# Optimization experiments

Hardware: AMD Instinct MI355X
Metric: run time of the kernel (lower is better)

The kernel has to match this reference:

```python
import jax, jax.numpy as jnp
import numpy as np

NEG_SLOPE_ATT = 0.2   # DenseGATConv default negative_slope
NEG_SLOPE_OUT = 0.01  # F.leaky_relu default


def dense_gat_layer(x, adj, w, att_src, att_dst, bias, heads, concat):
    # x: [B, N, F_in], adj: [B, N, N] (0/1 float), w: [F_in, H*C]
    B, N, _ = x.shape
    h = (x @ w).reshape(B, N, heads, -1)                 # [B, N, H, C]
    a_src = jnp.einsum('bnhc,hc->bnh', h, att_src)       # [B, N, H]
    a_dst = jnp.einsum('bnhc,hc->bnh', h, att_dst)       # [B, N, H]
    # alpha[b,i,j,h] = a_src[b,j,h] + a_dst[b,i,h]
    alpha = a_src[:, None, :, :] + a_dst[:, :, None, :]  # [B, N, N, H]
    alpha = jax.nn.leaky_relu(alpha, NEG_SLOPE_ATT)
    alpha = jnp.where(adj[..., None] == 0, -jnp.inf, alpha)
    alpha = jax.nn.softmax(alpha, axis=2)                # over neighbors j
    out = jnp.einsum('bijh,bjhc->bihc', alpha, h)        # [B, N, H, C]
    if concat:
        out = out.reshape(B, N, -1)                      # [B, N, H*C]
    else:
        out = out.mean(axis=2)                           # [B, N, C]
    return out + bias


def setup_inputs() -> dict:
    key = jax.random.key(0)
    ks = jax.random.split(key, 9)
    B, N, F_IN, HID, H1, OUT = 1, 4096, 256, 64, 8, 128
    x = jax.random.normal(ks[0], (B, N, F_IN), dtype=jnp.float32)
    u = jax.random.uniform(ks[1], (B, N, N), dtype=jnp.float32)
    adj = (u < 0.05).astype(jnp.float32)
    eye = jnp.eye(N, dtype=jnp.float32)[None]
    adj = jnp.maximum(adj, eye)  # ensure self-loop so softmax rows are valid
    s1 = 1.0 / np.sqrt(F_IN)
    s2 = 1.0 / np.sqrt(HID * H1)
    return {
        'x': x,
        'adj': adj,
        'w1': jax.random.normal(ks[2], (F_IN, H1 * HID), dtype=jnp.float32) * s1,
        'att_src1': jax.random.normal(ks[3], (H1, HID), dtype=jnp.float32) * s2,
        'att_dst1': jax.random.normal(ks[4], (H1, HID), dtype=jnp.float32) * s2,
        'b1': jnp.zeros((H1 * HID,), dtype=jnp.float32),
        'w2': jax.random.normal(ks[5], (H1 * HID, OUT), dtype=jnp.float32) * s2,
        'att_src2': jax.random.normal(ks[6], (1, OUT), dtype=jnp.float32) * 0.1,
        'att_dst2': jax.random.normal(ks[7], (1, OUT), dtype=jnp.float32) * 0.1,
        'b2': jnp.zeros((OUT,), dtype=jnp.float32),
    }


def reference(x, adj, w1, att_src1, att_dst1, b1, w2, att_src2, att_dst2, b2):
    h = dense_gat_layer(x, adj, w1, att_src1, att_dst1, b1, heads=8, concat=True)
    h = jax.nn.leaky_relu(h, NEG_SLOPE_OUT)
    h = dense_gat_layer(h, adj, w2, att_src2, att_dst2, b2, heads=1, concat=False)
    return jax.nn.leaky_relu(h, NEG_SLOPE_OUT)
```

## Files before the change

kernel.cpp:

```cpp
#include <hip/hip_runtime.h>
#include <hip/hip_bf16.h>
#include <cstdint>

#define N_NODES 4096
#define STRIDE  384
#define NPAIRS_MAX 192
#define QMAX    128
#define WROW    400

typedef _Float16 half2v __attribute__((ext_vector_type(2)));
typedef _Float16 v4h __attribute__((ext_vector_type(4)));
typedef _Float16 v8h __attribute__((ext_vector_type(8)));
typedef float    v4f __attribute__((ext_vector_type(4)));

__device__ __forceinline__ float f16lo(unsigned u) {
    half2v h = __builtin_bit_cast(half2v, u); return (float)h.x;
}
__device__ __forceinline__ float f16hi(unsigned u) {
    half2v h = __builtin_bit_cast(half2v, u); return (float)h.y;
}
__device__ __forceinline__ unsigned pk_lo(unsigned a, unsigned b) {
    return __builtin_amdgcn_perm(b, a, 0x05040100u);
}
__device__ __forceinline__ unsigned pk_hi(unsigned a, unsigned b) {
    return __builtin_amdgcn_perm(b, a, 0x07060302u);
}
__device__ __forceinline__ float fdot2f(unsigned v, unsigned w, float acc) {
    return __builtin_amdgcn_fdot2(__builtin_bit_cast(half2v, v),
                                  __builtin_bit_cast(half2v, w), acc, false);
}
__device__ __forceinline__ float lrelu02(float s) { return (s > 0.f) ? s : 0.2f * s; }
__device__ __forceinline__ float lrelu01(float s) { return (s > 0.f) ? s : 0.01f * s; }

__global__ __launch_bounds__(256) void build_nbr_kernel(
    const float* __restrict__ adj, unsigned short* __restrict__ nbr,
    int* __restrict__ cnt) {
    const int i    = blockIdx.x;
    const int tid  = threadIdx.x;
    const int wv   = tid >> 6;
    const int lane = tid & 63;
    __shared__ unsigned short s_buf[4][QMAX];
    __shared__ int s_cnt[4];
    const float4* row = (const float4*)(adj + (size_t)i * N_NODES);
    int base = 0;
#pragma unroll
    for (int it = 0; it < 4; it++) {
        float4 v = row[wv * 256 + it * 64 + lane];
        float e4[4] = {v.x, v.y, v.z, v.w};
        unsigned long long m4[4];
#pragma unroll
        for (int e = 0; e < 4; e++) m4[e] = __ballot(e4[e] != 0.0f);
#pragma unroll
        for (int e = 0; e < 4; e++) {
            int prefix = __popcll(m4[e] & ((1ull << lane) - 1ull));
            int pos = base + prefix;
            if (e4[e] != 0.0f && pos < QMAX)
                s_buf[wv][pos] = (unsigned short)(wv * 1024 + (it * 64 + lane) * 4 + e);
            base += __popcll(m4[e]);
        }
    }
    if (lane == 0) s_cnt[wv] = (base < QMAX) ? base : QMAX;
    __syncthreads();
    const int c0 = s_cnt[0], c1 = s_cnt[1], c2 = s_cnt[2], c3 = s_cnt[3];
    const int o1 = c0, o2 = c0 + c1, o3 = o2 + c2;
    int total = o3 + c3;
    if (total > STRIDE) total = STRIDE;
    for (int k = tid; k < total; k += 256) {
        int w, loc;
        if      (k < o1) { w = 0; loc = k; }
        else if (k < o2) { w = 1; loc = k - o1; }
        else if (k < o3) { w = 2; loc = k - o2; }
        else             { w = 3; loc = k - o3; }
        nbr[(size_t)i * STRIDE + k] = s_buf[w][loc];
    }
    if (tid == 0) cnt[i] = total;
}

__global__ __launch_bounds__(256) void prep_kernel(
    const float* __restrict__ x, const float* __restrict__ w1,
    const float* __restrict__ w2, _Float16* __restrict__ x16,
    _Float16* __restrict__ w1T, _Float16* __restrict__ w2T) {
    const int b = blockIdx.x, t = threadIdx.x;
    if (b < 1024) {
        const int idx = b * 1024 + t * 4;
        float4 v = *(const float4*)(x + idx);
        v4h h = { (_Float16)v.x, (_Float16)v.y, (_Float16)v.z, (_Float16)v.w };
        *(v4h*)(x16 + idx) = h;
    } else if (b < 1536) {
        const int idx = (b - 1024) * 256 + t;
        const int n = idx >> 8, k = idx & 255;
        w1T[idx] = (_Float16)w1[k * 512 + n];
    } else {
        const int idx = (b - 1536) * 256 + t;
        const int n = idx >> 9, k = idx & 511;
        w2T[idx] = (_Float16)w2[k * 128 + n];
    }
}

template<int KCH, int NSUB, int H>
__global__ __launch_bounds__(256) void gemm_mfma_kernel(
    const _Float16* __restrict__ A16, const _Float16* __restrict__ BT16,
    _Float16* __restrict__ C16,
    const float* __restrict__ att_s, const float* __restrict__ att_d,
    float* __restrict__ as_, float* __restrict__ ad_, int N) {
    const int K    = KCH * 32;
    const int wid  = blockIdx.x * 4 + (threadIdx.x >> 6);
    const int lane = threadIdx.x & 63;
    const int quad = lane >> 4, l16 = lane & 15;
    const int ntiles = N / (16 * NSUB);
    const int m0 = (wid / ntiles) * 16;
    const int n0 = (wid % ntiles) * (16 * NSUB);

    v8h a[KCH];
    const v8h* arow = (const v8h*)(A16 + (size_t)(m0 + l16) * K + quad * 8);
#pragma unroll
    for (int c = 0; c < KCH; c++) a[c] = arow[c * 4];

    float ps[4] = {}, pd[4] = {};
#pragma unroll
    for (int s = 0; s < NSUB; s++) {
        const int n = n0 + s * 16 + l16;
        const v8h* brow = (const v8h*)(BT16 + (size_t)n * K + quad * 8);
        v4f acc = {0.f, 0.f, 0.f, 0.f};
#pragma unroll
        for (int c = 0; c < KCH; c++)
            acc = __builtin_amdgcn_mfma_f32_16x16x32_f16(a[c], brow[c * 4], acc, 0, 0, 0);
        const float sa = att_s[n], sd = att_d[n];
#pragma unroll
        for (int r = 0; r < 4; r++) {
            C16[(size_t)(m0 + quad * 4 + r) * N + n] = (_Float16)acc[r];
            ps[r] += acc[r] * sa;
            pd[r] += acc[r] * sd;
        }
    }
#pragma unroll
    for (int r = 0; r < 4; r++) {
#pragma unroll
        for (int off = 1; off < 16; off <<= 1) {
            ps[r] += __shfl_xor(ps[r], off);
            pd[r] += __shfl_xor(pd[r], off);
        }
    }
    if (l16 == 0) {
        const int head = (H > 1) ? (n0 >> 6) : 0;
#pragma unroll
        for (int r = 0; r < 4; r++) {
            const int row = m0 + quad * 4 + r;
            as_[row * H + head] = ps[r];
            ad_[row * H + head] = pd[r];
        }
    }
}

__global__ __launch_bounds__(128) void attn1_kernel(
    const _Float16* __restrict__ h1g, const float* __restrict__ asrc,
    const float* __restrict__ adst, const unsigned short* __restrict__ nbr,
    const int* __restrict__ cnt, const float* __restrict__ b1,
    _Float16* __restrict__ out1f16) {
    const int i    = blockIdx.x;
    const int wv   = threadIdx.x >> 6;
    const int lane = threadIdx.x & 63;
    const int hd   = lane >> 3;
    __shared__ __align__(16) unsigned s_nb[NPAIRS_MAX];
    __shared__ __align__(16) unsigned short s_w16[8][WROW];
    __shared__ __align__(16) float s_comb[512];

    const int n      = cnt[i];
    const int npairs = (n + 1) >> 1;
    const int nq     = (npairs + 3) >> 2;
    const int npadp  = nq * 4;
    const int npadE  = npadp * 2;

    const unsigned* nbr32 = (const unsigned*)(nbr + (size_t)i * STRIDE);
    for (int k = lane; k < npadp; k += 64) {
        unsigned v = 0u;
        if (2 * k + 1 < n)  v = nbr32[k];
        else if (2 * k < n) v = nbr32[k] & 0xffffu;
        s_nb[k] = v;
    }

    float ad8[8];
    {
        const float4 a0 = *(const float4*)(adst + i * 8);
        const float4 a1 = *(const float4*)(adst + i * 8 + 4);
        ad8[0]=a0.x; ad8[1]=a0.y; ad8[2]=a0.z; ad8[3]=a0.w;
        ad8[4]=a1.x; ad8[5]=a1.y; ad8[6]=a1.z; ad8[7]=a1.w;
    }
    float m8[8];
#pragma unroll
    for (int k = 0; k < 8; k++) m8[k] = -1e30f;
    for (int e = lane; e < n; e += 64) {
        const int id = (s_nb[e >> 1] >> ((e & 1) * 16)) & 0xffff;
        const float4 q0 = *(const float4*)(asrc + id * 8);
        const float4 q1 = *(const float4*)(asrc + id * 8 + 4);
        const float sv[8] = {q0.x, q0.y, q0.z, q0.w, q1.x, q1.y, q1.z, q1.w};
#pragma unroll
        for (int k = 0; k < 8; k++) m8[k] = fmaxf(m8[k], lrelu02(sv[k] + ad8[k]));
    }
#pragma unroll
    for (int k = 0; k < 8; k++)
#pragma unroll
        for (int off = 32; off; off >>= 1) m8[k] = fmaxf(m8[k], __shfl_xor(m8[k], off));

    float l8[8];
#pragma unroll
    for (int k = 0; k < 8; k++) l8[k] = 0.f;
    for (int e = lane; e < npadE; e += 64) {
        if (e < n) {
            const int id = (s_nb[e >> 1] >> ((e & 1) * 16)) & 0xffff;
            const float4 q0 = *(const float4*)(asrc + id * 8);
            const float4 q1 = *(const float4*)(asrc + id * 8 + 4);
            const float sv[8] = {q0.x, q0.y, q0.z, q0.w, q1.x, q1.y, q1.z, q1.w};
#pragma unroll
            for (int k = 0; k < 8; k++) {
                float ev = __expf(lrelu02(sv[k] + ad8[k]) - m8[k]);
                _Float16 h = (_Float16)ev;
                l8[k] += (float)h;
                s_w16[k][e] = __builtin_bit_cast(unsigned short, h);
            }
        } else {
#pragma unroll
            for (int k = 0; k < 8; k++) s_w16[k][e] = 0;
        }
    }
#pragma unroll
    for (int k = 0; k < 8; k++)
#pragma unroll
        for (int off = 32; off; off >>= 1) l8[k] += __shfl_xor(l8[k], off);

    const char* hb = (const char*)h1g + lane * 16;
    float ac[8] = {};
    for (int q = wv; q < nq; q += 2) {
        const uint4 idq = *(const uint4*)&s_nb[q * 4];
        const uint4 wq  = *(const uint4*)((const unsigned*)&s_w16[hd][0] + q * 4);
        const unsigned idv[4] = {idq.x, idq.y, idq.z, idq.w};
        const unsigned wv4[4] = {wq.x, wq.y, wq.z, wq.w};
#pragma unroll
        for (int p = 0; p < 4; p++) {
            const int iA = idv[p] & 0xffff, iB = idv[p] >> 16;
            const uint4 vA = *(const uint4*)(hb + (size_t)iA * 1024);
            const uint4 vB = *(const uint4*)(hb + (size_t)iB * 1024);
            const unsigned w = wv4[p];
            ac[0] = fdot2f(pk_lo(vA.x, vB.x), w, ac[0]);
            ac[1] = fdot2f(pk_hi(vA.x, vB.x), w, ac[1]);
            ac[2] = fdot2f(pk_lo(vA.y, vB.y), w, ac[2]);
            ac[3] = fdot2f(pk_hi(vA.y, vB.y), w, ac[3]);
            ac[4] = fdot2f(pk_lo(vA.z, vB.z), w, ac[4]);
            ac[5] = fdot2f(pk_hi(vA.z, vB.z), w, ac[5]);
            ac[6] = fdot2f(pk_lo(vA.w, vB.w), w, ac[6]);
            ac[7] = fdot2f(pk_hi(vA.w, vB.w), w, ac[7]);
        }
    }
    if (wv == 0) {
        *(float4*)&s_comb[lane * 8]     = make_float4(ac[0], ac[1], ac[2], ac[3]);
        *(float4*)&s_comb[lane * 8 + 4] = make_float4(ac[4], ac[5], ac[6], ac[7]);
    }
    __syncthreads();
    if (wv == 1) {
        const float4 c0 = *(const float4*)&s_comb[lane * 8];
        const float4 c1 = *(const float4*)&s_comb[lane * 8 + 4];
        ac[0] += c0.x; ac[1] += c0.y; ac[2] += c0.z; ac[3] += c0.w;
        ac[4] += c1.x; ac[5] += c1.y; ac[6] += c1.z; ac[7] += c1.w;
        float lv = (hd < 4)
            ? ((hd < 2) ? (hd == 0 ? l8[0] : l8[1]) : (hd == 2 ? l8[2] : l8[3]))
            : ((hd < 6) ? (hd == 4 ? l8[4] : l8[5]) : (hd == 6 ? l8[6] : l8[7]));
        const float inv = 1.0f / lv;
        const float4 bb0 = *(const float4*)(b1 + lane * 8);
        const float4 bb1 = *(const float4*)(b1 + lane * 8 + 4);
        const float bbv[8] = {bb0.x, bb0.y, bb0.z, bb0.w, bb1.x, bb1.y, bb1.z, bb1.w};
        v8h ov;
#pragma unroll
        for (int c = 0; c < 8; c++)
            ov[c] = (_Float16)lrelu01(ac[c] * inv + bbv[c]);
        *(v8h*)(out1f16 + (size_t)i * 512 + lane * 8) = ov;
    }
}

__global__ __launch_bounds__(128) void attn2_kernel(
    const _Float16* __restrict__ h2g, const float* __restrict__ asrc,
    const float* __restrict__ adst, const unsigned short* __restrict__ nbr,
    const int* __restrict__ cnt, const float* __restrict__ b2,
    float* __restrict__ out) {
    const int wv   = threadIdx.x >> 6;
    const int i    = blockIdx.x * 2 + wv;
    const int lane = threadIdx.x & 63;
    const int grp  = lane >> 4, l16 = lane & 15;
    __shared__ __align__(16) unsigned s_nb[2][NPAIRS_MAX];
    __shared__ __align__(16) unsigned short s_w16[2][STRIDE + 16];

    const int n     = cnt[i];
    const int nq4   = (n + 3) >> 2;
    const int npad4 = nq4 * 4;
    const int npadp = (npad4 + 1) >> 1;

    const unsigned* nbr32 = (const unsigned*)(nbr + (size_t)i * STRIDE);
    for (int k = lane; k < npadp; k += 64) {
        unsigned v = 0u;
        if (2 * k + 1 < n)  v = nbr32[k];
        else if (2 * k < n) v = nbr32[k] & 0xffffu;
        s_nb[wv][k] = v;
    }

    const float ad = adst[i];
    float sreg[6];
    float m = -1e30f;
#pragma unroll
    for (int it = 0; it < 6; it++) {
        const int e = it * 64 + lane;
        float s = -1e30f;
        if (e < n) {
            const int id = (s_nb[wv][e >> 1] >> ((e & 1) * 16)) & 0xffff;
            s = lrelu02(asrc[id] + ad);
        }
        sreg[it] = s;
        m = fmaxf(m, s);
    }
#pragma unroll
    for (int off = 32; off; off >>= 1) m = fmaxf(m, __shfl_xor(m, off));
    float l = 0.f;
#pragma unroll
    for (int it = 0; it < 6; it++) {
        const int e = it * 64 + lane;
        if (e < n) {
            float ev = __expf(sreg[it] - m);
            _Float16 h = (_Float16)ev;
            l += (float)h;
            s_w16[wv][e] = __builtin_bit_cast(unsigned short, h);
        }
    }
    if (lane < npad4 - n) s_w16[wv][n + lane] = 0;
#pragma unroll
    for (int off = 32; off; off >>= 1) l += __shfl_xor(l, off);
    const float inv = 1.0f / l;

    const char* hb = (const char*)h2g + l16 * 16;
    float ac[8] = {};
    for (int it = 0; it < nq4; it++) {
        const int e = it * 4 + grp;
        const unsigned pr = s_nb[wv][e >> 1];
        const int id = (e & 1) ? (int)(pr >> 16) : (int)(pr & 0xffffu);
        const float w = (float)((const _Float16*)&s_w16[wv][0])[e];
        const uint4 v = *(const uint4*)(hb + (size_t)id * 256);
        ac[0] += w * f16lo(v.x); ac[1] += w * f16hi(v.x);
        ac[2] += w * f16lo(v.y); ac[3] += w * f16hi(v.y);
        ac[4] += w * f16lo(v.z); ac[5] += w * f16hi(v.z);
        ac[6] += w * f16lo(v.w); ac[7] += w * f16hi(v.w);
    }
#pragma unroll
    for (int c = 0; c < 8; c++) {
        ac[c] += __shfl_xor(ac[c], 16);
        ac[c] += __shfl_xor(ac[c], 32);
    }
    if (lane < 16) {
        const float4 bb0 = *(const float4*)(b2 + lane * 8);
        const float4 bb1 = *(const float4*)(b2 + lane * 8 + 4);
        float4 o0, o1;
        o0.x = lrelu01(ac[0] * inv + bb0.x);
        o0.y = lrelu01(ac[1] * inv + bb0.y);
        o0.z = lrelu01(ac[2] * inv + bb0.z);
        o0.w = lrelu01(ac[3] * inv + bb0.w);
        o1.x = lrelu01(ac[4] * inv + bb1.x);
        o1.y = lrelu01(ac[5] * inv + bb1.y);
        o1.z = lrelu01(ac[6] * inv + bb1.z);
        o1.w = lrelu01(ac[7] * inv + bb1.w);
        *(float4*)(out + (size_t)i * 128 + lane * 8)     = o0;
        *(float4*)(out + (size_t)i * 128 + lane * 8 + 4) = o1;
    }
}

extern "C" void kernel_launch(void* const* d_in, const int* in_sizes, int n_in,
                              void* d_out, int out_size, void* d_ws, size_t ws_size,
                              hipStream_t stream) {
    const float* x        = (const float*)d_in[0];
    const float* adj      = (const float*)d_in[1];
    const float* w1       = (const float*)d_in[2];
    const float* att_src1 = (const float*)d_in[3];
    const float* att_dst1 = (const float*)d_in[4];
    const float* b1       = (const float*)d_in[5];
    const float* w2       = (const float*)d_in[6];
    const float* att_src2 = (const float*)d_in[7];
    const float* att_dst2 = (const float*)d_in[8];
    const float* b2       = (const float*)d_in[9];
    float* out = (float*)d_out;

    float* ws   = (float*)d_ws;
    float* as1  = ws;
    float* ad1  = as1 + 4096 * 8;
    float* as2  = ad1 + 4096 * 8;
    float* ad2  = as2 + 4096;
    int*   cnt  = (int*)(ad2 + 4096);
    _Float16* x16   = (_Float16*)(cnt + 4096);
    _Float16* w1T   = x16 + (size_t)4096 * 256;
    _Float16* w2T   = w1T + 512 * 256;
    _Float16* h1g   = w2T + 128 * 512;
    _Float16* out1h = h1g + (size_t)4096 * 512;
    _Float16* h2g   = out1h + (size_t)4096 * 512;
    unsigned short* nbr = (unsigned short*)(h2g + (size_t)4096 * 128);

    build_nbr_kernel<<<N_NODES, 256, 0, stream>>>(adj, nbr, cnt);
    prep_kernel<<<1792, 256, 0, stream>>>(x, w1, w2, x16, w1T, w2T);

    gemm_mfma_kernel<8, 4, 8><<<512, 256, 0, stream>>>(
        x16, w1T, h1g, att_src1, att_dst1, as1, ad1, 512);
    attn1_kernel<<<N_NODES, 128, 0, stream>>>(h1g, as1, ad1, nbr, cnt, b1, out1h);

    gemm_mfma_kernel<16, 8, 1><<<64, 256, 0, stream>>>(
        out1h, w2T, h2g, att_src2, att_dst2, as2, ad2, 128);
    attn2_kernel<<<N_NODES / 2, 128, 0, stream>>>(h2g, as2, ad2, nbr, cnt, b2, out);
}
```

Baseline: 217.0 us.

## Fuse setup kernels, split GEMM2 columns with atomics, restructure attn1 partitioning

Merges the neighbor-list build and fp16 prep kernels into one launch, which also zeroes the layer-2 attention score buffers. GEMM2 moves from NSUB=8 over 64 blocks to NSUB=2 over 256 blocks, with the per-row attention dot products accumulated through atomicAdd. In attn1 each wave now computes its own max and sum over half the neighbors in contiguous chunks, and the halves are merged online-softmax style. The aggregation loop gets an 8-step unrolled block per wave. This removes one launch and raises GEMM2 parallelism, at the cost of atomics and some extra merge arithmetic.

```diff
diff --git a/kernel.cpp b/kernel.cpp
--- a/kernel.cpp
+++ b/kernel.cpp
@@ -32,68 +32,73 @@
 __device__ __forceinline__ float lrelu02(float s) { return (s > 0.f) ? s : 0.2f * s; }
 __device__ __forceinline__ float lrelu01(float s) { return (s > 0.f) ? s : 0.01f * s; }
 
-__global__ __launch_bounds__(256) void build_nbr_kernel(
+__global__ __launch_bounds__(256) void setup_kernel(
     const float* __restrict__ adj, unsigned short* __restrict__ nbr,
-    int* __restrict__ cnt) {
-    const int i    = blockIdx.x;
-    const int tid  = threadIdx.x;
-    const int wv   = tid >> 6;
-    const int lane = tid & 63;
-    __shared__ unsigned short s_buf[4][QMAX];
-    __shared__ int s_cnt[4];
-    const float4* row = (const float4*)(adj + (size_t)i * N_NODES);
-    int base = 0;
-#pragma unroll
-    for (int it = 0; it < 4; it++) {
-        float4 v = row[wv * 256 + it * 64 + lane];
-        float e4[4] = {v.x, v.y, v.z, v.w};
-        unsigned long long m4[4];
-#pragma unroll
-        for (int e = 0; e < 4; e++) m4[e] = __ballot(e4[e] != 0.0f);
-#pragma unroll
-        for (int e = 0; e < 4; e++) {
-            int prefix = __popcll(m4[e] & ((1ull << lane) - 1ull));
-            int pos = base + prefix;
-            if (e4[e] != 0.0f && pos < QMAX)
-                s_buf[wv][pos] = (unsigned short)(wv * 1024 + (it * 64 + lane) * 4 + e);
-            base += __popcll(m4[e]);
-        }
-    }
-    if (lane == 0) s_cnt[wv] = (base < QMAX) ? base : QMAX;
-    __syncthreads();
-    const int c0 = s_cnt[0], c1 = s_cnt[1], c2 = s_cnt[2], c3 = s_cnt[3];
-    const int o1 = c0, o2 = c0 + c1, o3 = o2 + c2;
-    int total = o3 + c3;
-    if (total > STRIDE) total = STRIDE;
-    for (int k = tid; k < total; k += 256) {
-        int w, loc;
-        if      (k < o1) { w = 0; loc = k; }
-        else if (k < o2) { w = 1; loc = k - o1; }
-        else if (k < o3) { w = 2; loc = k - o2; }
-        else             { w = 3; loc = k - o3; }
-        nbr[(size_t)i * STRIDE + k] = s_buf[w][loc];
-    }
-    if (tid == 0) cnt[i] = total;
-}
-
-__global__ __launch_bounds__(256) void prep_kernel(
+    int* __restrict__ cnt,
     const float* __restrict__ x, const float* __restrict__ w1,
     const float* __restrict__ w2, _Float16* __restrict__ x16,
-    _Float16* __restrict__ w1T, _Float16* __restrict__ w2T) {
+    _Float16* __restrict__ w1T, _Float16* __restrict__ w2T,
+    float* __restrict__ as2, float* __restrict__ ad2) {
     const int b = blockIdx.x, t = threadIdx.x;
-    if (b < 1024) {
-        const int idx = b * 1024 + t * 4;
+    if (b < 4096) {
+        const int i    = b;
+        const int wv   = t >> 6;
+        const int lane = t & 63;
+        __shared__ unsigned short s_buf[4][QMAX];
+        __shared__ int s_cnt[4];
+        const float4* row = (const float4*)(adj + (size_t)i * N_NODES);
+        int base = 0;
+#pragma unroll
+        for (int it = 0; it < 4; it++) {
+            float4 v = row[wv * 256 + it * 64 + lane];
+            float e4[4] = {v.x, v.y, v.z, v.w};
+            unsigned long long m4[4];
+#pragma unroll
+            for (int e = 0; e < 4; e++) m4[e] = __ballot(e4[e] != 0.0f);
+#pragma unroll
+            for (int e = 0; e < 4; e++) {
+                int prefix = __popcll(m4[e] & ((1ull << lane) - 1ull));
+                int pos = base + prefix;
+                if (e4[e] != 0.0f && pos < QMAX)
+                    s_buf[wv][pos] = (unsigned short)(wv * 1024 + (it * 64 + lane) * 4 + e);
+                base += __popcll(m4[e]);
+            }
+        }
+        if (lane == 0) s_cnt[wv] = (base < QMAX) ? base : QMAX;
+        __syncthreads();
+        const int c0 = s_cnt[0], c1 = s_cnt[1], c2 = s_cnt[2], c3 = s_cnt[3];
+        const int o1 = c0, o2 = c0 + c1, o3 = o2 + c2;
+        int total = o3 + c3;
+        if (total > STRIDE) total = STRIDE;
+        for (int k = t; k < total; k += 256) {
+            int w, loc;
+            if      (k < o1) { w = 0; loc = k; }
+            else if (k < o2) { w = 1; loc = k - o1; }
+            else if (k < o3) { w = 2; loc = k - o2; }
+            else             { w = 3; loc = k - o3; }
+            nbr[(size_t)i * STRIDE + k] = s_buf[w][loc];
+        }
+        if (t == 0) cnt[i] = total;
+    } else if (b < 5120) {
+        const int idx = (b - 4096) * 1024 + t * 4;
         float4 v = *(const float4*)(x + idx);
         v4h h = { (_Float16)v.x, (_Float16)v.y, (_Float16)v.z, (_Float16)v.w };
         *(v4h*)(x16 + idx) = h;
-    } else if (b < 1536) {
-        const int idx = (b - 1024) * 256 + t;
+    } else if (b < 5632) {
+        const int idx = (b - 5120) * 256 + t;
         const int n = idx >> 8, k = idx & 255;
         w1T[idx] = (_Float16)w1[k * 512 + n];
+    } else if (b < 5792) {
+        const int idx = (b - 5632) * 410;
+        const int e   = idx + t;
+        for (int q = e; q < idx + 410 && q < 65536; q += 256) {
+            const int n = q >> 9, k = q & 511;
+            w2T[q] = (_Float16)w2[k * 128 + n];
+        }
     } else {
-        const int idx = (b - 1536) * 256 + t;
-        const int n = idx >> 9, k = idx & 511;
-        w2T[idx] = (_Float16)w2[k * 128 + n];
+        const int idx = (b - 5792) * 256 + t;
+        as2[idx] = 0.f;
+        ad2[idx] = 0.f;
     }
 }
 
@@ -142,12 +147,17 @@
         }
     }
     if (l16 == 0) {
-        const int head = (H > 1) ? (n0 >> 6) : 0;
 #pragma unroll
         for (int r = 0; r < 4; r++) {
             const int row = m0 + quad * 4 + r;
-            as_[row * H + head] = ps[r];
-            ad_[row * H + head] = pd[r];
+            if (H > 1) {
+                const int head = n0 >> 6;
+                as_[row * H + head] = ps[r];
+                ad_[row * H + head] = pd[r];
+            } else {
+                atomicAdd(&as_[row], ps[r]);
+                atomicAdd(&ad_[row], pd[r]);
+            }
         }
     }
 }
@@ -164,6 +174,7 @@
     __shared__ __align__(16) unsigned s_nb[NPAIRS_MAX];
     __shared__ __align__(16) unsigned short s_w16[8][WROW];
     __shared__ __align__(16) float s_comb[512];
+    __shared__ float s_ml[2][2][8];
 
     const int n      = cnt[i];
     const int npairs = (n + 1) >> 1;
@@ -172,11 +183,14 @@
     const int npadE  = npadp * 2;
 
     const unsigned* nbr32 = (const unsigned*)(nbr + (size_t)i * STRIDE);
-    for (int k = lane; k < npadp; k += 64) {
-        unsigned v = 0u;
-        if (2 * k + 1 < n)  v = nbr32[k];
-        else if (2 * k < n) v = nbr32[k] & 0xffffu;
-        s_nb[k] = v;
+    for (int k0 = wv * 32; k0 < npadp; k0 += 128) {
+        const int k = k0 + (lane & 31) + ((lane >= 32) ? 64 : 0);
+        if (k < npadp) {
+            unsigned v = 0u;
+            if (2 * k + 1 < n)  v = nbr32[k];
+            else if (2 * k < n) v = nbr32[k] & 0xffffu;
+            s_nb[k] = v;
+        }
     }
 
     float ad8[8];
@@ -189,38 +203,44 @@
     float m8[8];
 #pragma unroll
     for (int k = 0; k < 8; k++) m8[k] = -1e30f;
-    for (int e = lane; e < n; e += 64) {
-        const int id = (s_nb[e >> 1] >> ((e & 1) * 16)) & 0xffff;
-        const float4 q0 = *(const float4*)(asrc + id * 8);
-        const float4 q1 = *(const float4*)(asrc + id * 8 + 4);
-        const float sv[8] = {q0.x, q0.y, q0.z, q0.w, q1.x, q1.y, q1.z, q1.w};
-#pragma unroll
-        for (int k = 0; k < 8; k++) m8[k] = fmaxf(m8[k], lrelu02(sv[k] + ad8[k]));
-    }
-#pragma unroll
-    for (int k = 0; k < 8; k++)
-#pragma unroll
-        for (int off = 32; off; off >>= 1) m8[k] = fmaxf(m8[k], __shfl_xor(m8[k], off));
-
-    float l8[8];
-#pragma unroll
-    for (int k = 0; k < 8; k++) l8[k] = 0.f;
-    for (int e = lane; e < npadE; e += 64) {
+    for (int e0 = wv * 64; e0 < n; e0 += 128) {
+        const int e = e0 + lane;
         if (e < n) {
             const int id = (s_nb[e >> 1] >> ((e & 1) * 16)) & 0xffff;
             const float4 q0 = *(const float4*)(asrc + id * 8);
             const float4 q1 = *(const float4*)(asrc + id * 8 + 4);
             const float sv[8] = {q0.x, q0.y, q0.z, q0.w, q1.x, q1.y, q1.z, q1.w};
 #pragma unroll
-            for (int k = 0; k < 8; k++) {
-                float ev = __expf(lrelu02(sv[k] + ad8[k]) - m8[k]);
-                _Float16 h = (_Float16)ev;
-                l8[k] += (float)h;
-                s_w16[k][e] = __builtin_bit_cast(unsigned short, h);
+            for (int k = 0; k < 8; k++) m8[k] = fmaxf(m8[k], lrelu02(sv[k] + ad8[k]));
+        }
+    }
+#pragma unroll
+    for (int k = 0; k < 8; k++)
+#pragma unroll
+        for (int off = 32; off; off >>= 1) m8[k] = fmaxf(m8[k], __shfl_xor(m8[k], off));
+
+    float l8[8];
+#pragma unroll
+    for (int k = 0; k < 8; k++) l8[k] = 0.f;
+    for (int e0 = wv * 64; e0 < npadE; e0 += 128) {
+        const int e = e0 + lane;
+        if (e < npadE) {
+            if (e < n) {
+                const int id = (s_nb[e >> 1] >> ((e & 1) * 16)) & 0xffff;
+                const float4 q0 = *(const float4*)(asrc + id * 8);
+                const float4 q1 = *(const float4*)(asrc + id * 8 + 4);
+                const float sv[8] = {q0.x, q0.y, q0.z, q0.w, q1.x, q1.y, q1.z, q1.w};
+#pragma unroll
+                for (int k = 0; k < 8; k++) {
+                    float ev = __expf(lrelu02(sv[k] + ad8[k]) - m8[k]);
+                    _Float16 h = (_Float16)ev;
+                    l8[k] += (float)h;
+                    s_w16[k][e] = __builtin_bit_cast(unsigned short, h);
+                }
+            } else {
+#pragma unroll
+                for (int k = 0; k < 8; k++) s_w16[k][e] = 0;
             }
-        } else {
-#pragma unroll
-            for (int k = 0; k < 8; k++) s_w16[k][e] = 0;
         }
     }
 #pragma unroll
@@ -230,48 +250,65 @@
 
     const char* hb = (const char*)h1g + lane * 16;
     float ac[8] = {};
-    for (int q = wv; q < nq; q += 2) {
-        const uint4 idq = *(const uint4*)&s_nb[q * 4];
-        const uint4 wq  = *(const uint4*)((const unsigned*)&s_w16[hd][0] + q * 4);
-        const unsigned idv[4] = {idq.x, idq.y, idq.z, idq.w};
-        const unsigned wv4[4] = {wq.x, wq.y, wq.z, wq.w};
-#pragma unroll
-        for (int p = 0; p < 4; p++) {
-            const int iA = idv[p] & 0xffff, iB = idv[p] >> 16;
-            const uint4 vA = *(const uint4*)(hb + (size_t)iA * 1024);
-            const uint4 vB = *(const uint4*)(hb + (size_t)iB * 1024);
-            const unsigned w = wv4[p];
-            ac[0] = fdot2f(pk_lo(vA.x, vB.x), w, ac[0]);
-            ac[1] = fdot2f(pk_hi(vA.x, vB.x), w, ac[1]);
-            ac[2] = fdot2f(pk_lo(vA.y, vB.y), w, ac[2]);
-            ac[3] = fdot2f(pk_hi(vA.y, vB.y), w, ac[3]);
-            ac[4] = fdot2f(pk_lo(vA.z, vB.z), w, ac[4]);
-            ac[5] = fdot2f(pk_hi(vA.z, vB.z), w, ac[5]);
-            ac[6] = fdot2f(pk_lo(vA.w, vB.w), w, ac[6]);
-            ac[7] = fdot2f(pk_hi(vA.w, vB.w), w, ac[7]);
+    for (int q0 = wv * 8; q0 < nq; q0 += 16) {
+#pragma unroll
+        for (int qq = 0; qq < 8; qq++) {
+            const int q = q0 + qq;
+            if (q >= nq) break;
+            const uint4 idq = *(const uint4*)&s_nb[q * 4];
+            const uint4 wq  = *(const uint4*)((const unsigned*)&s_w16[hd][0] + q * 4);
+            const unsigned idv[4] = {idq.x, idq.y, idq.z, idq.w};
+            const unsigned wv4[4] = {wq.x, wq.y, wq.z, wq.w};
+#pragma unroll
+            for (int p = 0; p < 4; p++) {
+                const int iA = idv[p] & 0xffff, iB = idv[p] >> 16;
+                const uint4 vA = *(const uint4*)(hb + (size_t)iA * 1024);
+                const uint4 vB = *(const uint4*)(hb + (size_t)iB * 1024);
+                const unsigned w = wv4[p];
+                ac[0] = fdot2f(pk_lo(vA.x, vB.x), w, ac[0]);
+                ac[1] = fdot2f(pk_hi(vA.x, vB.x), w, ac[1]);
+                ac[2] = fdot2f(pk_lo(vA.y, vB.y), w, ac[2]);
+                ac[3] = fdot2f(pk_hi(vA.y, vB.y), w, ac[3]);
+                ac[4] = fdot2f(pk_lo(vA.z, vB.z), w, ac[4]);
+                ac[5] = fdot2f(pk_hi(vA.z, vB.z), w, ac[5]);
+                ac[6] = fdot2f(pk_lo(vA.w, vB.w), w, ac[6]);
+                ac[7] = fdot2f(pk_hi(vA.w, vB.w), w, ac[7]);
+            }
         }
     }
     if (wv == 0) {
         *(float4*)&s_comb[lane * 8]     = make_float4(ac[0], ac[1], ac[2], ac[3]);
         *(float4*)&s_comb[lane * 8 + 4] = make_float4(ac[4], ac[5], ac[6], ac[7]);
     }
+    if (lane == 0) {
+#pragma unroll
+        for (int k = 0; k < 8; k++) {
+            s_ml[wv][0][k] = m8[k];
+            s_ml[wv][1][k] = l8[k];
+        }
+    }
     __syncthreads();
     if (wv == 1) {
+        const float m0v = s_ml[0][0][hd], l0v = s_ml[0][1][hd];
+        const float m1v = s_ml[1][0][hd], l1v = s_ml[1][1][hd];
+        const float mm = fmaxf(m0v, m1v);
+        const float a0s = __expf(m0v - mm), a1s = __expf(m1v - mm);
+        const float den = l0v * a0s + l1v * a1s;
+        const float inv = 1.0f / den;
         const float4 c0 = *(const float4*)&s_comb[lane * 8];
         const float4 c1 = *(const float4*)&s_comb[lane * 8 + 4];
-        ac[0] += c0.x; ac[1] += c0.y; ac[2] += c0.z; ac[3] += c0.w;
-        ac[4] += c1.x; ac[5] += c1.y; ac[6] += c1.z; ac[7] += c1.w;
-        float lv = (hd < 4)
-            ? ((hd < 2) ? (hd == 0 ? l8[0] : l8[1]) : (hd == 2 ? l8[2] : l8[3]))
-            : ((hd < 6) ? (hd == 4 ? l8[4] : l8[5]) : (hd == 6 ? l8[6] : l8[7]));
-        const float inv = 1.0f / lv;
+        const float o8[8] = {
+            c0.x * a0s + ac[0] * a1s, c0.y * a0s + ac[1] * a1s,
+            c0.z * a0s + ac[2] * a1s, c0.w * a0s + ac[3] * a1s,
+            c1.x * a0s + ac[4] * a1s, c1.y * a0s + ac[5] * a1s,
+            c1.z * a0s + ac[6] * a1s, c1.w * a0s + ac[7] * a1s };
         const float4 bb0 = *(const float4*)(b1 + lane * 8);
         const float4 bb1 = *(const float4*)(b1 + lane * 8 + 4);
         const float bbv[8] = {bb0.x, bb0.y, bb0.z, bb0.w, bb1.x, bb1.y, bb1.z, bb1.w};
         v8h ov;
 #pragma unroll
         for (int c = 0; c < 8; c++)
-            ov[c] = (_Float16)lrelu01(ac[c] * inv + bbv[c]);
+            ov[c] = (_Float16)lrelu01(o8[c] * inv + bbv[c]);
         *(v8h*)(out1f16 + (size_t)i * 512 + lane * 8) = ov;
     }
 }
@@ -397,14 +434,14 @@
     _Float16* h2g   = out1h + (size_t)4096 * 512;
     unsigned short* nbr = (unsigned short*)(h2g + (size_t)4096 * 128);
 
-    build_nbr_kernel<<<N_NODES, 256, 0, stream>>>(adj, nbr, cnt);
-    prep_kernel<<<1792, 256, 0, stream>>>(x, w1, w2, x16, w1T, w2T);
+    setup_kernel<<<5808, 256, 0, stream>>>(adj, nbr, cnt, x, w1, w2,
+                                           x16, w1T, w2T, as2, ad2);
 
     gemm_mfma_kernel<8, 4, 8><<<512, 256, 0, stream>>>(
         x16, w1T, h1g, att_src1, att_dst1, as1, ad1, 512);
     attn1_kernel<<<N_NODES, 128, 0, stream>>>(h1g, as1, ad1, nbr, cnt, b1, out1h);
 
-    gemm_mfma_kernel<16, 8, 1><<<64, 256, 0, stream>>>(
+    gemm_mfma_kernel<16, 2, 1><<<256, 256, 0, stream>>>(
         out1h, w2T, h2g, att_src2, att_dst2, as2, ad2, 128);
     attn2_kernel<<<N_NODES / 2, 128, 0, stream>>>(h2g, as2, ad2, nbr, cnt, b2, out);
 }
```

Measured after the change: 194.5 us. 1.12x faster.
